# Optimization experiments

Hardware: AMD Instinct MI355X
Metric: run time of the kernel (lower is better)

The kernel has to match this reference:

```python
import jax, jax.numpy as jnp
import numpy as np

B, L, S = 32, 128, 96
EMBED, HIDDEN = 768, 300
NUM_POS, NUM_DEP, NUM_REL = 50, 40, 41  # NUM_REL = num_dependencies + 1
NUM_LAYERS, NUM_LABEL = 2, 3


def setup_inputs() -> dict:
    key = jax.random.key(0)
    ks = jax.random.split(key, 12)
    text = jax.random.normal(ks[0], (B, L, EMBED), dtype=jnp.float32)
    context_masks = jnp.ones((B, L), dtype=jnp.int64)
    pos_tags = jax.random.randint(ks[1], (B, S), 0, NUM_POS)
    adjacency_tensors = jax.random.uniform(ks[2], (B, NUM_REL, S, S), dtype=jnp.float32)
    # learned parameters
    pos_emb = jax.random.normal(ks[3], (NUM_POS, EMBED), dtype=jnp.float32) * 0.02
    pos_emb = pos_emb.at[0].set(0.0)  # padding_idx=0
    lin_W = jax.random.normal(ks[4], (EMBED, HIDDEN), dtype=jnp.float32) * 0.02
    lin_b = jnp.zeros((HIDDEN,), dtype=jnp.float32)
    rgcn_W = jax.random.normal(ks[5], (NUM_LAYERS, NUM_REL, HIDDEN, HIDDEN), dtype=jnp.float32) * 0.05
    score_W = jax.random.normal(ks[6], (NUM_LAYERS, HIDDEN), dtype=jnp.float32) * 0.05
    score_b = jnp.zeros((NUM_LAYERS,), dtype=jnp.float32)
    dense_W = jax.random.normal(ks[7], (2 * HIDDEN, NUM_LABEL), dtype=jnp.float32) * 0.02
    dense_b = jnp.zeros((NUM_LABEL,), dtype=jnp.float32)
    return dict(text=text, context_masks=context_masks, pos_tags=pos_tags,
                adjacency_tensors=adjacency_tensors, pos_emb=pos_emb,
                lin_W=lin_W, lin_b=lin_b, rgcn_W=rgcn_W, score_W=score_W,
                score_b=score_b, dense_W=dense_W, dense_b=dense_b)


def rgcn_layer(x, adj, W, sw, sb):
    # x: [B,S,H], adj: [B,R,S,S], W: [R,H,H]
    hidden = jnp.einsum('bsi,rio->brso', x, W)           # per-relation transform
    denom = jnp.sum(adj, axis=3, keepdims=True)          # [B,R,S,1]
    intm = jnp.einsum('brst,brto->brso', adj, hidden)    # adjacency aggregation
    div = intm / jnp.where(denom == 0.0, 1.0, denom)     # safe normalize
    scores = jnp.einsum('brso,o->brs', div, sw) + sb     # relation attention logits
    r = jax.nn.softmax(scores, axis=1)                   # softmax over relations
    out = jnp.einsum('brso,brs->bso', div, r)            # weighted combine
    return jax.nn.relu(out)


def reference(text, context_masks, pos_tags, adjacency_tensors, pos_emb,
              lin_W, lin_b, rgcn_W, score_W, score_b, dense_W, dense_b):
    embedding_len = jnp.sum(context_masks, axis=-1).astype(jnp.float32)  # [B]
    text_out = text @ lin_W + lin_b                                      # embed_dim != hidden_dim path
    hc = text_out                                                        # [B,L,H]
    review_text_len = jnp.sum(pos_tags != 0, axis=-1).astype(jnp.float32)
    review = pos_emb[pos_tags] @ lin_W + lin_b                           # [B,S,H]
    hg = review
    for l in range(NUM_LAYERS):
        hg = rgcn_layer(hg, adjacency_tensors, rgcn_W[l], score_W[l], score_b[l])
    hc_mean = jnp.sum(hc, axis=1) / embedding_len[:, None]
    hg_mean = jnp.sum(hg, axis=1) / review_text_len[:, None]
    final_x = jnp.concatenate([hg_mean, hc_mean], axis=-1)
    return final_x @ dense_W + dense_b                                   # [B, num_label]
```

## Files before the change

kernel.cpp:

```cpp
#include <hip/hip_runtime.h>

#define NB 32
#define NLEN 128
#define NS 96
#define NE 768
#define NH 300
#define NR 41

#define OFF_TSUM   0u
#define OFF_ELEN   24576u
#define OFF_RLEN   24608u
#define OFF_HCM    24640u
#define OFF_TAB    34240u
#define OFF_HGA    49240u
#define OFF_HGB    970840u
#define OFF_SWT    1892440u
#define OFF_U      1904740u
#define OFF_SPRE   2030692u
#define OFF_RDEN   2156644u
#define OFF_C      2282596u
#define OFF_M      2408548u

__device__ __forceinline__ float wave_reduce(float v) {
#pragma unroll
  for (int off = 32; off > 0; off >>= 1) v += __shfl_down(v, off);
  return v;
}

__global__ void k_tsum(const float* __restrict__ text, float* __restrict__ tsum) {
  int b = blockIdx.x;
  int tid = threadIdx.x;
  for (int e = tid; e < NE; e += 256) {
    const float* p = text + (size_t)b * NLEN * NE + e;
    float s = 0.f;
#pragma unroll 4
    for (int l = 0; l < NLEN; ++l) s += p[(size_t)l * NE];
    tsum[b * NE + e] = s;
  }
}

__global__ void k_len(const int* __restrict__ cm, const int* __restrict__ pt,
                      float* __restrict__ elen, float* __restrict__ rlen) {
  int b = threadIdx.x;
  if (b < NB) {
    int s1 = 0;
    for (int l = 0; l < NLEN; ++l) s1 += cm[b * NLEN + l];
    int s2 = 0;
    for (int s = 0; s < NS; ++s) s2 += (pt[b * NS + s] != 0) ? 1 : 0;
    elen[b] = (float)s1;
    rlen[b] = (float)s2;
  }
}

__global__ void k_hcmean(const float* __restrict__ tsum, const float* __restrict__ linW,
                         const float* __restrict__ linb, const float* __restrict__ elen,
                         float* __restrict__ hcm) {
  int idx = blockIdx.x * 256 + threadIdx.x;
  if (idx >= NB * NH) return;
  int b = idx / NH, h = idx - b * NH;
  const float* tp = tsum + b * NE;
  float s = 0.f;
  for (int e = 0; e < NE; ++e) s += tp[e] * linW[(size_t)e * NH + h];
  hcm[idx] = (s + (float)NLEN * linb[h]) / elen[b];
}

__global__ void k_table(const float* __restrict__ pemb, const float* __restrict__ linW,
                        const float* __restrict__ linb, float* __restrict__ tab) {
  int idx = blockIdx.x * 256 + threadIdx.x;
  if (idx >= 50 * NH) return;
  int p = idx / NH, h = idx - p * NH;
  const float* pp = pemb + (size_t)p * NE;
  float s = 0.f;
  for (int e = 0; e < NE; ++e) s += pp[e] * linW[(size_t)e * NH + h];
  tab[idx] = s + linb[h];
}

__global__ void k_gather(const int* __restrict__ pt, const float* __restrict__ tab,
                         float* __restrict__ hg) {
  int idx = blockIdx.x * 256 + threadIdx.x;
  if (idx >= NB * NS * NH) return;
  int h = idx % NH;
  int bs = idx / NH;
  hg[idx] = tab[pt[bs] * NH + h];
}

__global__ void k_swt(const float* __restrict__ Wl, const float* __restrict__ sw,
                      float* __restrict__ swt) {
  int gw = (blockIdx.x * blockDim.x + threadIdx.x) >> 6;
  int lane = threadIdx.x & 63;
  if (gw >= NR * NH) return;
  const float* wp = Wl + (size_t)gw * NH;
  float s = 0.f;
  for (int o = lane; o < NH; o += 64) s += wp[o] * sw[o];
  s = wave_reduce(s);
  if (lane == 0) swt[gw] = s;
}

__global__ void k_u(const float* __restrict__ x, const float* __restrict__ swt,
                    float* __restrict__ u) {
  int gw = (blockIdx.x * blockDim.x + threadIdx.x) >> 6;
  int lane = threadIdx.x & 63;
  if (gw >= NB * NR * NS) return;
  int t = gw % NS;
  int br = gw / NS;
  int r = br % NR;
  int b = br / NR;
  const float* xp = x + (size_t)(b * NS + t) * NH;
  const float* sp = swt + (size_t)r * NH;
  float s = 0.f;
  for (int i = lane; i < NH; i += 64) s += xp[i] * sp[i];
  s = wave_reduce(s);
  if (lane == 0) u[gw] = s;
}

__global__ void k_scores(const float* __restrict__ adj, const float* __restrict__ u,
                         const float* __restrict__ sb, float* __restrict__ spre,
                         float* __restrict__ rden) {
  int gw = (blockIdx.x * blockDim.x + threadIdx.x) >> 6;
  int lane = threadIdx.x & 63;
  if (gw >= NB * NR * NS) return;
  int s = gw % NS;
  int br = gw / NS;
  int r = br % NR;
  int b = br / NR;
  const float* ap = adj + (size_t)gw * NS;
  const float* up = u + (size_t)br * NS;
  float d = 0.f, v = 0.f;
  for (int t = lane; t < NS; t += 64) {
    float a = ap[t];
    d += a;
    v += a * up[t];
  }
  d = wave_reduce(d);
  v = wave_reduce(v);
  if (lane == 0) {
    float ds = (d == 0.f) ? 1.f : d;
    int o = (b * NS + s) * NR + r;
    spre[o] = v / ds + sb[0];
    rden[o] = 1.f / ds;
  }
}

__global__ void k_softmax(const float* __restrict__ spre, const float* __restrict__ rden,
                          float* __restrict__ c) {
  int bs = blockIdx.x * 256 + threadIdx.x;
  if (bs >= NB * NS) return;
  int b = bs / NS, s = bs - b * NS;
  float vals[NR];
  float m = -1e30f;
#pragma unroll
  for (int r = 0; r < NR; ++r) {
    vals[r] = spre[(size_t)bs * NR + r];
    m = fmaxf(m, vals[r]);
  }
  float sum = 0.f;
#pragma unroll
  for (int r = 0; r < NR; ++r) {
    float e = expf(vals[r] - m);
    vals[r] = e;
    sum += e;
  }
  float inv = 1.f / sum;
#pragma unroll
  for (int r = 0; r < NR; ++r) {
    c[((size_t)(b * NR + r)) * NS + s] = vals[r] * inv * rden[(size_t)bs * NR + r];
  }
}

__global__ __launch_bounds__(384)
void k_pmat(const float* __restrict__ adj, const float* __restrict__ x,
            const float* __restrict__ c, float* __restrict__ M,
            int r0, int rgn) {
  __shared__ float At[96 * 100];
  __shared__ float Xl[96 * 68];
  const int tid = threadIdx.x;
  int bid = blockIdx.x;
  const int ic = bid % 5; bid /= 5;
  const int rg = bid % rgn;
  const int b = bid / rgn;
  const int r = r0 + rg;
  const int i0 = ic << 6;
  const int iw = (i0 + 64 <= NH) ? 64 : (NH - i0);

  const float* ap = adj + (size_t)(b * NR + r) * NS * NS;
  for (int idx = tid; idx < NS * NS; idx += 384) {
    int s = idx / 96, t = idx - s * 96;
    At[t * 100 + s] = ap[idx];
  }
  const float* xp = x + (size_t)b * NS * NH;
  for (int idx = tid; idx < 96 * 64; idx += 384) {
    int t = idx >> 6, ii = idx & 63;
    Xl[t * 68 + ii] = (ii < iw) ? xp[(size_t)t * NH + i0 + ii] : 0.f;
  }
  __syncthreads();

  const int sg = tid % 24;
  const int ig = tid / 24;
  const int s0 = sg << 2;
  const int ii0 = ig << 2;
  float acc[4][4] = {};
#pragma unroll 4
  for (int t = 0; t < 96; ++t) {
    float4 av = *(const float4*)&At[t * 100 + s0];
    float4 xv = *(const float4*)&Xl[t * 68 + ii0];
    float as[4] = {av.x, av.y, av.z, av.w};
    float xs[4] = {xv.x, xv.y, xv.z, xv.w};
#pragma unroll
    for (int i = 0; i < 4; ++i)
#pragma unroll
      for (int j = 0; j < 4; ++j)
        acc[i][j] += as[i] * xs[j];
  }

  if (ii0 < iw) {
    const size_t Kst = (size_t)rgn * NH;
#pragma unroll
    for (int i = 0; i < 4; ++i) {
      int s = s0 + i;
      float cc = c[(size_t)(b * NR + r) * NS + s];
      float* mp = M + ((size_t)(b * NS) + s) * Kst + (size_t)rg * NH + i0 + ii0;
      mp[0] = acc[i][0] * cc;
      mp[1] = acc[i][1] * cc;
      mp[2] = acc[i][2] * cc;
      mp[3] = acc[i][3] * cc;
    }
  }
}

__global__ __launch_bounds__(256)
void k_gemm(const float* __restrict__ A, const float* __restrict__ Bw,
            float* __restrict__ y, int K, int first, int last) {
  __shared__ float Al[2][32 * 68];
  __shared__ float Bl[2][32 * 68];
  const int tid = threadIdx.x;
  const int row0 = blockIdx.x << 6;
  const int o0 = blockIdx.y << 6;
  const int rg = tid & 15;
  const int og = tid >> 4;
  float acc[4][4] = {};
  float ra[8], rb[8];
  const int nt = (K + 31) >> 5;

#pragma unroll
  for (int j = 0; j < 8; ++j) {
    int idx = tid + (j << 8);
    int ridx = idx >> 5, kk = idx & 31;
    ra[j] = (kk < K) ? A[(size_t)(row0 + ridx) * K + kk] : 0.f;
    int kb = idx >> 6, oo = idx & 63;
    int oc = o0 + oo;
    rb[j] = (kb < K && oc < NH) ? Bw[(size_t)kb * NH + oc] : 0.f;
  }
#pragma unroll
  for (int j = 0; j < 8; ++j) {
    int idx = tid + (j << 8);
    Al[0][(idx & 31) * 68 + (idx >> 5)] = ra[j];
    Bl[0][(idx >> 6) * 68 + (idx & 63)] = rb[j];
  }
  __syncthreads();

  for (int tI = 0; tI < nt; ++tI) {
    int cur = tI & 1;
    if (tI + 1 < nt) {
      int kt = (tI + 1) << 5;
#pragma unroll
      for (int j = 0; j < 8; ++j) {
        int idx = tid + (j << 8);
        int ridx = idx >> 5, kk = kt + (idx & 31);
        ra[j] = (kk < K) ? A[(size_t)(row0 + ridx) * K + kk] : 0.f;
        int kb = kt + (idx >> 6), oo = idx & 63;
        int oc = o0 + oo;
        rb[j] = (kb < K && oc < NH) ? Bw[(size_t)kb * NH + oc] : 0.f;
      }
    }
    const float* Ac = Al[cur];
    const float* Bc = Bl[cur];
#pragma unroll
    for (int kk = 0; kk < 32; ++kk) {
      float4 av = *(const float4*)&Ac[kk * 68 + (rg << 2)];
      float4 bv = *(const float4*)&Bc[kk * 68 + (og << 2)];
      float as[4] = {av.x, av.y, av.z, av.w};
      float bs[4] = {bv.x, bv.y, bv.z, bv.w};
#pragma unroll
      for (int i = 0; i < 4; ++i)
#pragma unroll
        for (int j = 0; j < 4; ++j)
          acc[i][j] += as[i] * bs[j];
    }
    __syncthreads();
    if (tI + 1 < nt) {
      int nxt = cur ^ 1;
#pragma unroll
      for (int j = 0; j < 8; ++j) {
        int idx = tid + (j << 8);
        Al[nxt][(idx & 31) * 68 + (idx >> 5)] = ra[j];
        Bl[nxt][(idx >> 6) * 68 + (idx & 63)] = rb[j];
      }
      __syncthreads();
    }
  }

#pragma unroll
  for (int i = 0; i < 4; ++i) {
    int row = row0 + (rg << 2) + i;
#pragma unroll
    for (int j = 0; j < 4; ++j) {
      int col = o0 + (og << 2) + j;
      if (col < NH) {
        size_t off = (size_t)row * NH + col;
        float v = acc[i][j];
        if (!first) v += y[off];
        if (last) v = fmaxf(v, 0.f);
        y[off] = v;
      }
    }
  }
}

__global__ void k_final(const float* __restrict__ hg, const float* __restrict__ rlen,
                        const float* __restrict__ hcm, const float* __restrict__ dW,
                        const float* __restrict__ db, float* __restrict__ out) {
  int b = blockIdx.x;
  __shared__ float hgm[NH];
  int tid = threadIdx.x;
  for (int h = tid; h < NH; h += 256) {
    float s = 0.f;
    for (int ss = 0; ss < NS; ++ss) s += hg[((size_t)(b * NS) + ss) * NH + h];
    hgm[h] = s / rlen[b];
  }
  __syncthreads();
  if (tid < 3) {
    float s = db[tid];
    for (int h = 0; h < NH; ++h) s += hgm[h] * dW[h * 3 + tid];
    for (int h = 0; h < NH; ++h) s += hcm[b * NH + h] * dW[(NH + h) * 3 + tid];
    out[b * 3 + tid] = s;
  }
}

extern "C" void kernel_launch(void* const* d_in, const int* in_sizes, int n_in,
                              void* d_out, int out_size, void* d_ws, size_t ws_size,
                              hipStream_t stream) {
  (void)in_sizes; (void)n_in; (void)out_size;
  const float* text   = (const float*)d_in[0];
  const int*   cmask  = (const int*)d_in[1];
  const int*   ptags  = (const int*)d_in[2];
  const float* adj    = (const float*)d_in[3];
  const float* pemb   = (const float*)d_in[4];
  const float* linW   = (const float*)d_in[5];
  const float* linb   = (const float*)d_in[6];
  const float* rgcnW  = (const float*)d_in[7];
  const float* scoreW = (const float*)d_in[8];
  const float* scoreB = (const float*)d_in[9];
  const float* denseW = (const float*)d_in[10];
  const float* denseB = (const float*)d_in[11];
  float* out = (float*)d_out;
  float* ws = (float*)d_ws;

  float* tsum = ws + OFF_TSUM;
  float* elen = ws + OFF_ELEN;
  float* rlen = ws + OFF_RLEN;
  float* hcm  = ws + OFF_HCM;
  float* tab  = ws + OFF_TAB;
  float* hgA  = ws + OFF_HGA;
  float* hgB  = ws + OFF_HGB;
  float* swt  = ws + OFF_SWT;
  float* ubuf = ws + OFF_U;
  float* spre = ws + OFF_SPRE;
  float* rden = ws + OFF_RDEN;
  float* cbuf = ws + OFF_C;
  float* Mbuf = ws + OFF_M;

  size_t avail = ws_size / sizeof(float);
  size_t mcap = (avail > OFF_M) ? (avail - OFF_M) : 0;
  int RG = (int)(mcap / ((size_t)NB * NS * NH));
  if (RG > NR) RG = NR;
  if (RG < 1) RG = 1;

  k_tsum<<<dim3(NB), dim3(256), 0, stream>>>(text, tsum);
  k_len<<<dim3(1), dim3(64), 0, stream>>>(cmask, ptags, elen, rlen);
  k_hcmean<<<dim3((NB * NH + 255) / 256), dim3(256), 0, stream>>>(tsum, linW, linb, elen, hcm);
  k_table<<<dim3((50 * NH + 255) / 256), dim3(256), 0, stream>>>(pemb, linW, linb, tab);
  k_gather<<<dim3((NB * NS * NH + 255) / 256), dim3(256), 0, stream>>>(ptags, tab, hgA);

  float* x = hgA;
  float* yb = hgB;
  for (int l = 0; l < 2; ++l) {
    const float* Wl = rgcnW + (size_t)l * NR * NH * NH;
    k_swt<<<dim3((NR * NH) / 4), dim3(256), 0, stream>>>(Wl, scoreW + l * NH, swt);
    k_u<<<dim3((NB * NR * NS) / 4), dim3(256), 0, stream>>>(x, swt, ubuf);
    k_scores<<<dim3((NB * NR * NS) / 4), dim3(256), 0, stream>>>(adj, ubuf, scoreB + l, spre, rden);
    k_softmax<<<dim3((NB * NS + 255) / 256), dim3(256), 0, stream>>>(spre, rden, cbuf);
    int ng = (NR + RG - 1) / RG;
    for (int g = 0; g < ng; ++g) {
      int r0 = g * RG;
      int rgn = (r0 + RG <= NR) ? RG : (NR - r0);
      k_pmat<<<dim3(NB * rgn * 5), dim3(384), 0, stream>>>(adj, x, cbuf, Mbuf, r0, rgn);
      k_gemm<<<dim3(48, 5), dim3(256), 0, stream>>>(Mbuf, Wl + (size_t)r0 * NH * NH, yb,
                                                    rgn * NH, (g == 0) ? 1 : 0,
                                                    (g == ng - 1) ? 1 : 0);
    }
    float* tswap = x; x = yb; yb = tswap;
  }
  k_final<<<dim3(NB), dim3(256), 0, stream>>>(x, rlen, hcm, denseW, denseB, out);
}
```

Before: 2.363 ms.

## Fuse per-relation transform and adjacency aggregation into one kernel with split-relation reduction

```diff
diff --git a/kernel.cpp b/kernel.cpp
--- a/kernel.cpp
+++ b/kernel.cpp
@@ -6,6 +6,9 @@
 #define NE 768
 #define NH 300
 #define NR 41
+#define RCH 7
+#define RPC 6
+#define OCT 5
 
 #define OFF_TSUM   0u
 #define OFF_ELEN   24576u
@@ -19,7 +22,9 @@
 #define OFF_SPRE   2030692u
 #define OFF_RDEN   2156644u
 #define OFF_C      2282596u
-#define OFF_M      2408548u
+#define OFF_P      2408548u
+
+__device__ __forceinline__ int SW(int o) { return o + ((o >> 5) << 2); }
 
 __device__ __forceinline__ float wave_reduce(float v) {
 #pragma unroll
@@ -167,153 +172,163 @@
   }
 }
 
-__global__ __launch_bounds__(384)
-void k_pmat(const float* __restrict__ adj, const float* __restrict__ x,
-            const float* __restrict__ c, float* __restrict__ M,
-            int r0, int rgn) {
-  __shared__ float At[96 * 100];
-  __shared__ float Xl[96 * 68];
+__global__ __launch_bounds__(192)
+void k_fused(const float* __restrict__ adj, const float* __restrict__ x,
+             const float* __restrict__ cbuf, const float* __restrict__ Wl,
+             float* __restrict__ P) {
+  __shared__ __align__(16) float sA[32 * 108];
+  __shared__ __align__(16) float sB[32 * 68];
+  __shared__ __align__(16) float sH[96 * 68];
+
   const int tid = threadIdx.x;
   int bid = blockIdx.x;
-  const int ic = bid % 5; bid /= 5;
-  const int rg = bid % rgn;
-  const int b = bid / rgn;
-  const int r = r0 + rg;
-  const int i0 = ic << 6;
-  const int iw = (i0 + 64 <= NH) ? 64 : (NH - i0);
-
-  const float* ap = adj + (size_t)(b * NR + r) * NS * NS;
-  for (int idx = tid; idx < NS * NS; idx += 384) {
-    int s = idx / 96, t = idx - s * 96;
-    At[t * 100 + s] = ap[idx];
-  }
-  const float* xp = x + (size_t)b * NS * NH;
-  for (int idx = tid; idx < 96 * 64; idx += 384) {
-    int t = idx >> 6, ii = idx & 63;
-    Xl[t * 68 + ii] = (ii < iw) ? xp[(size_t)t * NH + i0 + ii] : 0.f;
-  }
-  __syncthreads();
-
-  const int sg = tid % 24;
-  const int ig = tid / 24;
-  const int s0 = sg << 2;
-  const int ii0 = ig << 2;
-  float acc[4][4] = {};
-#pragma unroll 4
-  for (int t = 0; t < 96; ++t) {
-    float4 av = *(const float4*)&At[t * 100 + s0];
-    float4 xv = *(const float4*)&Xl[t * 68 + ii0];
-    float as[4] = {av.x, av.y, av.z, av.w};
-    float xs[4] = {xv.x, xv.y, xv.z, xv.w};
+  const int oc = bid % OCT; bid /= OCT;
+  const int rg = bid % RCH;
+  const int b = bid / RCH;
+  const int o0 = oc * 64;
+  const int r0 = rg * RPC;
+  const int nr = (r0 + RPC <= NR) ? RPC : (NR - r0);
+
+  const int g1 = tid >> 3;
+  const int g2 = tid & 7;
+  const int fa = SW(g1 * 4);
+  const int fb = SW(g2 * 8);
+
+  float accO[4][8];
+#pragma unroll
+  for (int i = 0; i < 4; ++i)
+#pragma unroll
+    for (int j = 0; j < 8; ++j) accO[i][j] = 0.f;
+
+  const float* xb = x + (size_t)b * NS * NH;
+
+  for (int rr = 0; rr < nr; ++rr) {
+    const int r = r0 + rr;
+    const float* wp = Wl + (size_t)r * NH * NH;
+    const float* ap = adj + (size_t)(b * NR + r) * NS * NS;
+    const float* cp = cbuf + (size_t)(b * NR + r) * NS;
+
+    float acc1[4][8];
 #pragma unroll
     for (int i = 0; i < 4; ++i)
 #pragma unroll
-      for (int j = 0; j < 4; ++j)
-        acc[i][j] += as[i] * xs[j];
-  }
-
-  if (ii0 < iw) {
-    const size_t Kst = (size_t)rgn * NH;
-#pragma unroll
-    for (int i = 0; i < 4; ++i) {
-      int s = s0 + i;
-      float cc = c[(size_t)(b * NR + r) * NS + s];
-      float* mp = M + ((size_t)(b * NS) + s) * Kst + (size_t)rg * NH + i0 + ii0;
-      mp[0] = acc[i][0] * cc;
-      mp[1] = acc[i][1] * cc;
-      mp[2] = acc[i][2] * cc;
-      mp[3] = acc[i][3] * cc;
-    }
-  }
-}
-
-__global__ __launch_bounds__(256)
-void k_gemm(const float* __restrict__ A, const float* __restrict__ Bw,
-            float* __restrict__ y, int K, int first, int last) {
-  __shared__ float Al[2][32 * 68];
-  __shared__ float Bl[2][32 * 68];
-  const int tid = threadIdx.x;
-  const int row0 = blockIdx.x << 6;
-  const int o0 = blockIdx.y << 6;
-  const int rg = tid & 15;
-  const int og = tid >> 4;
-  float acc[4][4] = {};
-  float ra[8], rb[8];
-  const int nt = (K + 31) >> 5;
-
-#pragma unroll
-  for (int j = 0; j < 8; ++j) {
-    int idx = tid + (j << 8);
-    int ridx = idx >> 5, kk = idx & 31;
-    ra[j] = (kk < K) ? A[(size_t)(row0 + ridx) * K + kk] : 0.f;
-    int kb = idx >> 6, oo = idx & 63;
-    int oc = o0 + oo;
-    rb[j] = (kb < K && oc < NH) ? Bw[(size_t)kb * NH + oc] : 0.f;
-  }
-#pragma unroll
-  for (int j = 0; j < 8; ++j) {
-    int idx = tid + (j << 8);
-    Al[0][(idx & 31) * 68 + (idx >> 5)] = ra[j];
-    Bl[0][(idx >> 6) * 68 + (idx & 63)] = rb[j];
-  }
-  __syncthreads();
-
-  for (int tI = 0; tI < nt; ++tI) {
-    int cur = tI & 1;
-    if (tI + 1 < nt) {
-      int kt = (tI + 1) << 5;
-#pragma unroll
-      for (int j = 0; j < 8; ++j) {
-        int idx = tid + (j << 8);
-        int ridx = idx >> 5, kk = kt + (idx & 31);
-        ra[j] = (kk < K) ? A[(size_t)(row0 + ridx) * K + kk] : 0.f;
-        int kb = kt + (idx >> 6), oo = idx & 63;
-        int oc = o0 + oo;
-        rb[j] = (kb < K && oc < NH) ? Bw[(size_t)kb * NH + oc] : 0.f;
+      for (int j = 0; j < 8; ++j) acc1[i][j] = 0.f;
+
+    for (int kc = 0; kc < 10; ++kc) {
+      const int k0 = kc * 32;
+      __syncthreads();
+#pragma unroll
+      for (int p = 0; p < 4; ++p) {
+        int idx = tid + p * 192;
+        int kq = (idx & 7) * 4;
+        int t = idx >> 3;
+        int k = k0 + kq;
+        float4 v = make_float4(0.f, 0.f, 0.f, 0.f);
+        if (k + 3 < NH) v = *(const float4*)&xb[t * NH + k];
+        int col = SW(t);
+        sA[(kq + 0) * 108 + col] = v.x;
+        sA[(kq + 1) * 108 + col] = v.y;
+        sA[(kq + 2) * 108 + col] = v.z;
+        sA[(kq + 3) * 108 + col] = v.w;
+      }
+#pragma unroll
+      for (int p = 0; p < 3; ++p) {
+        int idx = tid + p * 192;
+        if (idx < 512) {
+          int oq = (idx & 15) * 4;
+          int kk = idx >> 4;
+          int k = k0 + kk;
+          int o = o0 + oq;
+          float4 v = make_float4(0.f, 0.f, 0.f, 0.f);
+          if (k < NH) {
+            const float* wrow = wp + (size_t)k * NH;
+            v.x = (o + 0 < NH) ? wrow[o + 0] : 0.f;
+            v.y = (o + 1 < NH) ? wrow[o + 1] : 0.f;
+            v.z = (o + 2 < NH) ? wrow[o + 2] : 0.f;
+            v.w = (o + 3 < NH) ? wrow[o + 3] : 0.f;
+          }
+          *(float4*)&sB[kk * 68 + SW(oq)] = v;
+        }
+      }
+      __syncthreads();
+#pragma unroll
+      for (int kk = 0; kk < 32; ++kk) {
+        float4 a = *(const float4*)&sA[kk * 108 + fa];
+        float4 b0 = *(const float4*)&sB[kk * 68 + fb];
+        float4 b1 = *(const float4*)&sB[kk * 68 + fb + 4];
+        float as[4] = {a.x, a.y, a.z, a.w};
+        float bs[8] = {b0.x, b0.y, b0.z, b0.w, b1.x, b1.y, b1.z, b1.w};
+#pragma unroll
+        for (int i = 0; i < 4; ++i)
+#pragma unroll
+          for (int j = 0; j < 8; ++j) acc1[i][j] += as[i] * bs[j];
       }
     }
-    const float* Ac = Al[cur];
-    const float* Bc = Bl[cur];
-#pragma unroll
-    for (int kk = 0; kk < 32; ++kk) {
-      float4 av = *(const float4*)&Ac[kk * 68 + (rg << 2)];
-      float4 bv = *(const float4*)&Bc[kk * 68 + (og << 2)];
-      float as[4] = {av.x, av.y, av.z, av.w};
-      float bs[4] = {bv.x, bv.y, bv.z, bv.w};
-#pragma unroll
-      for (int i = 0; i < 4; ++i)
-#pragma unroll
-        for (int j = 0; j < 4; ++j)
-          acc[i][j] += as[i] * bs[j];
+
+#pragma unroll
+    for (int i = 0; i < 4; ++i) {
+      float4 h0 = make_float4(acc1[i][0], acc1[i][1], acc1[i][2], acc1[i][3]);
+      float4 h1 = make_float4(acc1[i][4], acc1[i][5], acc1[i][6], acc1[i][7]);
+      *(float4*)&sH[(g1 * 4 + i) * 68 + fb] = h0;
+      *(float4*)&sH[(g1 * 4 + i) * 68 + fb + 4] = h1;
     }
-    __syncthreads();
-    if (tI + 1 < nt) {
-      int nxt = cur ^ 1;
-#pragma unroll
-      for (int j = 0; j < 8; ++j) {
-        int idx = tid + (j << 8);
-        Al[nxt][(idx & 31) * 68 + (idx >> 5)] = ra[j];
-        Bl[nxt][(idx >> 6) * 68 + (idx & 63)] = rb[j];
+
+    for (int tc = 0; tc < 3; ++tc) {
+      const int t0 = tc * 32;
+      __syncthreads();
+#pragma unroll
+      for (int p = 0; p < 4; ++p) {
+        int idx = tid + p * 192;
+        int tq = (idx & 7) * 4;
+        int s = idx >> 3;
+        float4 v = *(const float4*)&ap[s * NS + t0 + tq];
+        float cs = cp[s];
+        int col = SW(s);
+        sA[(tq + 0) * 108 + col] = v.x * cs;
+        sA[(tq + 1) * 108 + col] = v.y * cs;
+        sA[(tq + 2) * 108 + col] = v.z * cs;
+        sA[(tq + 3) * 108 + col] = v.w * cs;
       }
       __syncthreads();
-    }
-  }
-
-#pragma unroll
-  for (int i = 0; i < 4; ++i) {
-    int row = row0 + (rg << 2) + i;
-#pragma unroll
-    for (int j = 0; j < 4; ++j) {
-      int col = o0 + (og << 2) + j;
-      if (col < NH) {
-        size_t off = (size_t)row * NH + col;
-        float v = acc[i][j];
-        if (!first) v += y[off];
-        if (last) v = fmaxf(v, 0.f);
-        y[off] = v;
+#pragma unroll
+      for (int kk = 0; kk < 32; ++kk) {
+        float4 a = *(const float4*)&sA[kk * 108 + fa];
+        float4 b0 = *(const float4*)&sH[(t0 + kk) * 68 + fb];
+        float4 b1 = *(const float4*)&sH[(t0 + kk) * 68 + fb + 4];
+        float as[4] = {a.x, a.y, a.z, a.w};
+        float bs[8] = {b0.x, b0.y, b0.z, b0.w, b1.x, b1.y, b1.z, b1.w};
+#pragma unroll
+        for (int i = 0; i < 4; ++i)
+#pragma unroll
+          for (int j = 0; j < 8; ++j) accO[i][j] += as[i] * bs[j];
       }
     }
   }
+
+  float* pp = P + ((size_t)rg * NB + b) * NS * NH;
+#pragma unroll
+  for (int i = 0; i < 4; ++i) {
+    int s = g1 * 4 + i;
+    int o = o0 + g2 * 8;
+    float* row = pp + (size_t)s * NH + o;
+    if (o + 7 < NH) {
+      *(float4*)&row[0] = make_float4(accO[i][0], accO[i][1], accO[i][2], accO[i][3]);
+      *(float4*)&row[4] = make_float4(accO[i][4], accO[i][5], accO[i][6], accO[i][7]);
+    } else {
+#pragma unroll
+      for (int j = 0; j < 8; ++j)
+        if (o + j < NH) row[j] = accO[i][j];
+    }
+  }
+}
+
+__global__ void k_reduce(const float* __restrict__ P, float* __restrict__ y) {
+  int idx = blockIdx.x * 256 + threadIdx.x;
+  if (idx >= NB * NS * NH) return;
+  float s = 0.f;
+#pragma unroll
+  for (int ch = 0; ch < RCH; ++ch) s += P[(size_t)ch * (NB * NS * NH) + idx];
+  y[idx] = fmaxf(s, 0.f);
 }
 
 __global__ void k_final(const float* __restrict__ hg, const float* __restrict__ rlen,
@@ -339,7 +354,7 @@
 extern "C" void kernel_launch(void* const* d_in, const int* in_sizes, int n_in,
                               void* d_out, int out_size, void* d_ws, size_t ws_size,
                               hipStream_t stream) {
-  (void)in_sizes; (void)n_in; (void)out_size;
+  (void)in_sizes; (void)n_in; (void)out_size; (void)ws_size;
   const float* text   = (const float*)d_in[0];
   const int*   cmask  = (const int*)d_in[1];
   const int*   ptags  = (const int*)d_in[2];
@@ -367,13 +382,7 @@
   float* spre = ws + OFF_SPRE;
   float* rden = ws + OFF_RDEN;
   float* cbuf = ws + OFF_C;
-  float* Mbuf = ws + OFF_M;
-
-  size_t avail = ws_size / sizeof(float);
-  size_t mcap = (avail > OFF_M) ? (avail - OFF_M) : 0;
-  int RG = (int)(mcap / ((size_t)NB * NS * NH));
-  if (RG > NR) RG = NR;
-  if (RG < 1) RG = 1;
+  float* Pbuf = ws + OFF_P;
 
   k_tsum<<<dim3(NB), dim3(256), 0, stream>>>(text, tsum);
   k_len<<<dim3(1), dim3(64), 0, stream>>>(cmask, ptags, elen, rlen);
@@ -389,15 +398,8 @@
     k_u<<<dim3((NB * NR * NS) / 4), dim3(256), 0, stream>>>(x, swt, ubuf);
     k_scores<<<dim3((NB * NR * NS) / 4), dim3(256), 0, stream>>>(adj, ubuf, scoreB + l, spre, rden);
     k_softmax<<<dim3((NB * NS + 255) / 256), dim3(256), 0, stream>>>(spre, rden, cbuf);
-    int ng = (NR + RG - 1) / RG;
-    for (int g = 0; g < ng; ++g) {
-      int r0 = g * RG;
-      int rgn = (r0 + RG <= NR) ? RG : (NR - r0);
-      k_pmat<<<dim3(NB * rgn * 5), dim3(384), 0, stream>>>(adj, x, cbuf, Mbuf, r0, rgn);
-      k_gemm<<<dim3(48, 5), dim3(256), 0, stream>>>(Mbuf, Wl + (size_t)r0 * NH * NH, yb,
-                                                    rgn * NH, (g == 0) ? 1 : 0,
-                                                    (g == ng - 1) ? 1 : 0);
-    }
+    k_fused<<<dim3(NB * RCH * OCT), dim3(192), 0, stream>>>(adj, x, cbuf, Wl, Pbuf);
+    k_reduce<<<dim3((NB * NS * NH + 255) / 256), dim3(256), 0, stream>>>(Pbuf, yb);
     float* tswap = x; x = yb; yb = tswap;
   }
   k_final<<<dim3(NB), dim3(256), 0, stream>>>(x, rlen, hcm, denseW, denseB, out);
```

Result: faster. 2.087 ms (-11.7%).
